# Kernel optimization log

Hardware: AMD Instinct MI355X
Metric: run time of the kernel (lower is better)

Reference implementation:

```python
import jax, jax.numpy as jnp
import numpy as np

B = 64            # number of graphs
NPG = 64          # nodes per graph (static; lengths are all equal here)
N = B * NPG       # total nodes = sum(lengths)
LT = 128          # max text tokens per node
LL = 32           # max labels per node
VOCAB = 50000
TOTAL_NUM = 100000
D = 256           # embedding_text == embedding_label == hidden_dimension
OUT = 1024


def setup_inputs() -> dict:
    key = jax.random.key(0)
    ks = jax.random.split(key, 12)
    return {
        "text_ids": jax.random.randint(ks[0], (N, LT), 0, VOCAB),
        "label_ids": jax.random.randint(ks[1], (N, LL), 0, TOTAL_NUM),
        "text_len": jax.random.randint(ks[2], (N,), 1, LT + 1),
        "label_len": jax.random.randint(ks[3], (N,), 1, LL + 1),
        "word_emb": jax.random.normal(ks[4], (VOCAB, D), jnp.float32) * 0.02,
        "label_emb": jax.random.normal(ks[5], (TOTAL_NUM, D), jnp.float32) * 0.02,
        "Wg_text": jax.random.normal(ks[6], (D, D), jnp.float32) * (1.0 / np.sqrt(D)),
        "Wg_label": jax.random.normal(ks[7], (D, D), jnp.float32) * (1.0 / np.sqrt(D)),
        "w_adap": jax.random.normal(ks[8], (2,), jnp.float32),
        "W1": jax.random.normal(ks[9], (D, D), jnp.float32) * (1.0 / np.sqrt(D)),
        "b1": jnp.zeros((D,), jnp.float32),
        "Wout": jax.random.normal(ks[10], (D, OUT), jnp.float32) * (1.0 / np.sqrt(D)),
        "bout": jnp.zeros((OUT,), jnp.float32),
    }


def _ragged_bag(table, ids, lens, mean):
    # gather rows then masked sum over the ragged axis (EmbeddingBag-style)
    L = ids.shape[1]
    mask = (jnp.arange(L)[None, :] < lens[:, None]).astype(table.dtype)  # [N, L]
    emb = table[ids]                                                     # [N, L, D]
    out = jnp.einsum("nld,nl->nd", emb, mask)
    if mean:
        out = out / lens[:, None].astype(table.dtype)
    return out


def reference(text_ids, label_ids, text_len, label_len, word_emb, label_emb,
              Wg_text, Wg_label, w_adap, W1, b1, Wout, bout):
    # fetchFeature: per-node ragged mean of word embeddings, ragged sum of label embeddings
    text_out = _ragged_bag(word_emb, text_ids, text_len, mean=True)    # [N, D]
    label_out = _ragged_bag(label_emb, label_ids, label_len, mean=False)  # [N, D]

    # weighted_GCN surrogate: per-type linear projection + relu, then per-graph mean readout
    h_t = jax.nn.relu(text_out @ Wg_text)   # [N, D]
    h_l = jax.nn.relu(label_out @ Wg_label)  # [N, D]
    seg = jnp.repeat(jnp.arange(B), NPG)     # graph id per node
    r_t = jax.ops.segment_sum(h_t, seg, num_segments=B) / NPG  # [B, D]
    r_l = jax.ops.segment_sum(h_l, seg, num_segments=B) / NPG  # [B, D]

    # adap: Linear(2,1,bias=False) over stacked (text,label), then MLLinear fusion
    fused = jnp.stack([r_t, r_l], axis=-1) @ w_adap  # [B, D]
    h = jax.nn.relu(fused @ W1 + b1)
    return h @ Wout + bout  # [B, OUT]
```

## Files before the change

### kernel.cpp

```cpp
#include <hip/hip_runtime.h>

#define NN      4096
#define BG      64
#define NPG_    64
#define LT_     128
#define LL_     32
#define D_      256
#define OUT_    1024

typedef __attribute__((ext_vector_type(8))) short bf16x8;
typedef __attribute__((ext_vector_type(4))) float f32x4;

__device__ __forceinline__ void split_bf16(float v, unsigned short& hi, unsigned short& lo) {
    union { float f; unsigned u; } a; a.f = v;
    const unsigned hu = (a.u + 0x8000u) & 0xFFFF0000u;
    union { unsigned u; float f; } h; h.u = hu;
    const float r = v - h.f;
    union { float f; unsigned u; } b; b.f = r;
    hi = (unsigned short)(hu >> 16);
    lo = (unsigned short)(((b.u + 0x8000u) & 0xFFFF0000u) >> 16);
}

__global__ __launch_bounds__(256) void convw_kernel(
    const float* __restrict__ Wg_text,
    const float* __restrict__ Wg_label,
    unsigned short* __restrict__ Wpk)
{
    const int b   = blockIdx.x;
    const int mat = b >> 7;
    const int nt  = (b >> 3) & 15;
    const int ks  = b & 7;
    const float* __restrict__ W = mat ? Wg_label : Wg_text;
    const int tid = threadIdx.x;

    #pragma unroll
    for (int r = 0; r < 2; ++r) {
        const int idx = tid + 256 * r;
        const int kl  = idx >> 4;
        const int c16 = idx & 15;
        const int k   = ks * 32 + kl;
        const float v = W[(size_t)k * D_ + nt * 16 + c16];
        unsigned short h, l;
        split_bf16(v, h, l);
        const int lane = c16 + 16 * ((kl >> 3) & 3);
        const int e    = kl & 7;
        const size_t bh = ((((size_t)mat * 2 + 0) * 16 + nt) * 8 + ks) * 512 + lane * 8 + e;
        const size_t bl = ((((size_t)mat * 2 + 1) * 16 + nt) * 8 + ks) * 512 + lane * 8 + e;
        Wpk[bh] = h;
        Wpk[bl] = l;
    }
}

__global__ __launch_bounds__(256) void gather_kernel(
    const int*   __restrict__ text_ids,
    const int*   __restrict__ label_ids,
    const int*   __restrict__ text_len,
    const int*   __restrict__ label_len,
    const float* __restrict__ word_emb,
    const float* __restrict__ label_emb,
    unsigned short* __restrict__ xh_t,
    unsigned short* __restrict__ xl_t,
    unsigned short* __restrict__ xh_l,
    unsigned short* __restrict__ xl_l)
{
    __shared__ int   sIds[LT_ + LL_];
    __shared__ float redT[4][D_];
    __shared__ float redL[4][D_];

    const int n    = blockIdx.x;
    const int tid  = threadIdx.x;
    const int wave = tid >> 6;
    const int lane = tid & 63;

    if (tid < LT_)               sIds[tid] = text_ids [(size_t)n * LT_ + tid];
    else if (tid < LT_ + LL_)    sIds[tid] = label_ids[(size_t)n * LL_ + (tid - LT_)];
    const int lt = text_len[n];
    const int ll = label_len[n];
    __syncthreads();

    float4 aT = make_float4(0.f, 0.f, 0.f, 0.f);
    float4 aL = make_float4(0.f, 0.f, 0.f, 0.f);

    {
        const float* __restrict__ bp = word_emb + (size_t)lane * 4;
        #pragma unroll 8
        for (int l = wave; l < lt; l += 4) {
            const float4 v = *reinterpret_cast<const float4*>(bp + (size_t)sIds[l] * D_);
            aT.x += v.x; aT.y += v.y; aT.z += v.z; aT.w += v.w;
        }
    }
    {
        const float* __restrict__ bp = label_emb + (size_t)lane * 4;
        #pragma unroll 8
        for (int l = wave; l < ll; l += 4) {
            const float4 v = *reinterpret_cast<const float4*>(bp + (size_t)sIds[LT_ + l] * D_);
            aL.x += v.x; aL.y += v.y; aL.z += v.z; aL.w += v.w;
        }
    }

    *reinterpret_cast<float4*>(&redT[wave][lane * 4]) = aT;
    *reinterpret_cast<float4*>(&redL[wave][lane * 4]) = aL;
    __syncthreads();

    const float t  = ((redT[0][tid] + redT[1][tid]) + (redT[2][tid] + redT[3][tid])) / (float)lt;
    const float lv =  (redL[0][tid] + redL[1][tid]) + (redL[2][tid] + redL[3][tid]);

    unsigned short h, l;
    const size_t o = (size_t)n * D_ + tid;
    split_bf16(t,  h, l);  xh_t[o] = h;  xl_t[o] = l;
    split_bf16(lv, h, l);  xh_l[o] = h;  xl_l[o] = l;
}

__global__ __launch_bounds__(512) void proj_kernel(
    const unsigned short* __restrict__ xh_t,
    const unsigned short* __restrict__ xl_t,
    const unsigned short* __restrict__ xh_l,
    const unsigned short* __restrict__ xl_l,
    const unsigned short* __restrict__ Wpk,
    const float* __restrict__ w_adap,
    float*       __restrict__ h_comb)
{
    __shared__ __align__(16) short ldsX[4][16 * D_];

    const int tid  = threadIdx.x;
    const int wave = tid >> 6;
    const int lane = tid & 63;
    const int base = blockIdx.x * 16;

    {
        const int nd = tid >> 5, ch = tid & 31;
        const size_t g = (size_t)(base + nd) * D_ + ch * 8;
        const int d = nd * D_ + ((ch ^ (nd & 7)) * 8);
        *reinterpret_cast<int4*>(&ldsX[0][d]) = *reinterpret_cast<const int4*>(&xh_t[g]);
        *reinterpret_cast<int4*>(&ldsX[1][d]) = *reinterpret_cast<const int4*>(&xl_t[g]);
        *reinterpret_cast<int4*>(&ldsX[2][d]) = *reinterpret_cast<const int4*>(&xh_l[g]);
        *reinterpret_cast<int4*>(&ldsX[3][d]) = *reinterpret_cast<const int4*>(&xl_l[g]);
    }
    __syncthreads();

    const int nt0 = wave * 2;
    const int row = lane & 15;
    const int kc  = lane >> 4;
    f32x4 accT[2] = {{0.f,0.f,0.f,0.f},{0.f,0.f,0.f,0.f}};
    f32x4 accL[2] = {{0.f,0.f,0.f,0.f},{0.f,0.f,0.f,0.f}};

    #pragma unroll
    for (int ks = 0; ks < 8; ++ks) {
        const int aidx = row * D_ + (((ks * 4 + kc) ^ (row & 7)) * 8);
        const bf16x8 ath  = *reinterpret_cast<const bf16x8*>(&ldsX[0][aidx]);
        const bf16x8 atl  = *reinterpret_cast<const bf16x8*>(&ldsX[1][aidx]);
        const bf16x8 alh  = *reinterpret_cast<const bf16x8*>(&ldsX[2][aidx]);
        const bf16x8 all_ = *reinterpret_cast<const bf16x8*>(&ldsX[3][aidx]);

        #pragma unroll
        for (int i = 0; i < 2; ++i) {
            const int nt = nt0 + i;
            const bf16x8 bth = *reinterpret_cast<const bf16x8*>(
                &Wpk[(((size_t)0 * 16 + nt) * 8 + ks) * 512 + lane * 8]);
            const bf16x8 btl = *reinterpret_cast<const bf16x8*>(
                &Wpk[(((size_t)1 * 16 + nt) * 8 + ks) * 512 + lane * 8]);
            const bf16x8 blh = *reinterpret_cast<const bf16x8*>(
                &Wpk[(((size_t)2 * 16 + nt) * 8 + ks) * 512 + lane * 8]);
            const bf16x8 bll = *reinterpret_cast<const bf16x8*>(
                &Wpk[(((size_t)3 * 16 + nt) * 8 + ks) * 512 + lane * 8]);

            accT[i] = __builtin_amdgcn_mfma_f32_16x16x32_bf16(ath, bth, accT[i], 0, 0, 0);
            accT[i] = __builtin_amdgcn_mfma_f32_16x16x32_bf16(ath, btl, accT[i], 0, 0, 0);
            accT[i] = __builtin_amdgcn_mfma_f32_16x16x32_bf16(atl, bth, accT[i], 0, 0, 0);
            accT[i] = __builtin_amdgcn_mfma_f32_16x16x32_bf16(atl, btl, accT[i], 0, 0, 0);

            accL[i] = __builtin_amdgcn_mfma_f32_16x16x32_bf16(alh, blh, accL[i], 0, 0, 0);
            accL[i] = __builtin_amdgcn_mfma_f32_16x16x32_bf16(alh, bll, accL[i], 0, 0, 0);
            accL[i] = __builtin_amdgcn_mfma_f32_16x16x32_bf16(all_, blh, accL[i], 0, 0, 0);
            accL[i] = __builtin_amdgcn_mfma_f32_16x16x32_bf16(all_, bll, accL[i], 0, 0, 0);
        }
    }

    const float w0r = w_adap[0] * (1.0f / (float)NPG_);
    const float w1r = w_adap[1] * (1.0f / (float)NPG_);
    #pragma unroll
    for (int i = 0; i < 2; ++i) {
        #pragma unroll
        for (int r = 0; r < 4; ++r) {
            const int node = base + kc * 4 + r;
            const int col  = (nt0 + i) * 16 + row;
            const float ht = accT[i][r] > 0.f ? accT[i][r] : 0.f;
            const float hl = accL[i][r] > 0.f ? accL[i][r] : 0.f;
            h_comb[(size_t)node * D_ + col] = w0r * ht + w1r * hl;
        }
    }
}

__global__ __launch_bounds__(256) void graph_kernel(
    const float* __restrict__ h_comb,
    const float* __restrict__ W1,
    const float* __restrict__ b1,
    const float* __restrict__ Wout,
    const float* __restrict__ bout,
    float*       __restrict__ out)
{
    __shared__ float fused[D_];
    __shared__ float hrow[D_];

    const int bx   = blockIdx.x;
    const int b    = bx >> 2;
    const int part = bx & 3;
    const int tid  = threadIdx.x;

    float acc = 0.f;
    const float* __restrict__ basep = h_comb + (size_t)b * NPG_ * D_ + tid;
    #pragma unroll 8
    for (int n = 0; n < NPG_; ++n) acc += basep[(size_t)n * D_];
    fused[tid] = acc;
    __syncthreads();

    float a1 = b1[tid];
    for (int d = 0; d < D_; ++d)
        a1 = fmaf(fused[d], W1[(size_t)d * D_ + tid], a1);
    hrow[tid] = a1 > 0.f ? a1 : 0.f;
    __syncthreads();

    const int j = part * 256 + tid;
    float o = bout[j];
    for (int d = 0; d < D_; ++d)
        o = fmaf(hrow[d], Wout[(size_t)d * OUT_ + j], o);
    out[(size_t)b * OUT_ + j] = o;
}

extern "C" void kernel_launch(void* const* d_in, const int* in_sizes, int n_in,
                              void* d_out, int out_size, void* d_ws, size_t ws_size,
                              hipStream_t stream) {
    const int*   text_ids  = (const int*)  d_in[0];
    const int*   label_ids = (const int*)  d_in[1];
    const int*   text_len  = (const int*)  d_in[2];
    const int*   label_len = (const int*)  d_in[3];
    const float* word_emb  = (const float*)d_in[4];
    const float* label_emb = (const float*)d_in[5];
    const float* Wg_text   = (const float*)d_in[6];
    const float* Wg_label  = (const float*)d_in[7];
    const float* w_adap    = (const float*)d_in[8];
    const float* W1        = (const float*)d_in[9];
    const float* b1        = (const float*)d_in[10];
    const float* Wout      = (const float*)d_in[11];
    const float* bout      = (const float*)d_in[12];

    char* ws = (char*)d_ws;
    float*          h_comb = (float*)ws;
    unsigned short* xh_t   = (unsigned short*)(ws + (4  << 20));
    unsigned short* xl_t   = (unsigned short*)(ws + (6  << 20));
    unsigned short* xh_l   = (unsigned short*)(ws + (8  << 20));
    unsigned short* xl_l   = (unsigned short*)(ws + (10 << 20));
    unsigned short* Wpk    = (unsigned short*)(ws + (12 << 20));
    float*          out    = (float*)d_out;

    convw_kernel<<<256, 256, 0, stream>>>(Wg_text, Wg_label, Wpk);

    gather_kernel<<<NN, 256, 0, stream>>>(
        text_ids, label_ids, text_len, label_len,
        word_emb, label_emb, xh_t, xl_t, xh_l, xl_l);

    proj_kernel<<<NN / 16, 512, 0, stream>>>(
        xh_t, xl_t, xh_l, xl_l, Wpk, w_adap, h_comb);

    graph_kernel<<<BG * 4, 256, 0, stream>>>(
        h_comb, W1, b1, Wout, bout, out);
}
```

Baseline: 88.83 us.

## Split proj kernel across column halves and drop low-low MFMA term

The projection kernel now launches twice as many blocks, each covering half the output columns with one 16-column tile per wave instead of two, which raises parallelism across CUs. It also removes the lo*lo product from the split-bf16 three-term emulation, cutting the MFMAs per tile from 8 to 6. A min-blocks hint is added to launch bounds. Each block still reloads the full 16-node input tile into LDS, so input reads double. Dropping the lo*lo term slightly reduces precision.

```diff
diff --git a/kernel.cpp b/kernel.cpp
--- a/kernel.cpp
+++ b/kernel.cpp
@@ -111,7 +111,7 @@
     split_bf16(lv, h, l);  xh_l[o] = h;  xl_l[o] = l;
 }
 
-__global__ __launch_bounds__(512) void proj_kernel(
+__global__ __launch_bounds__(512, 4) void proj_kernel(
     const unsigned short* __restrict__ xh_t,
     const unsigned short* __restrict__ xl_t,
     const unsigned short* __restrict__ xh_l,
@@ -122,10 +122,12 @@
 {
     __shared__ __align__(16) short ldsX[4][16 * D_];
 
-    const int tid  = threadIdx.x;
-    const int wave = tid >> 6;
-    const int lane = tid & 63;
-    const int base = blockIdx.x * 16;
+    const int tid   = threadIdx.x;
+    const int wave  = tid >> 6;
+    const int lane  = tid & 63;
+    const int ntile = blockIdx.x >> 1;
+    const int chalf = blockIdx.x & 1;
+    const int base  = ntile * 16;
 
     {
         const int nd = tid >> 5, ch = tid & 31;
@@ -138,11 +140,11 @@
     }
     __syncthreads();
 
-    const int nt0 = wave * 2;
+    const int nt  = chalf * 8 + wave;
     const int row = lane & 15;
     const int kc  = lane >> 4;
-    f32x4 accT[2] = {{0.f,0.f,0.f,0.f},{0.f,0.f,0.f,0.f}};
-    f32x4 accL[2] = {{0.f,0.f,0.f,0.f},{0.f,0.f,0.f,0.f}};
+    f32x4 accT = {0.f, 0.f, 0.f, 0.f};
+    f32x4 accL = {0.f, 0.f, 0.f, 0.f};
 
     #pragma unroll
     for (int ks = 0; ks < 8; ++ks) {
@@ -152,42 +154,33 @@
         const bf16x8 alh  = *reinterpret_cast<const bf16x8*>(&ldsX[2][aidx]);
         const bf16x8 all_ = *reinterpret_cast<const bf16x8*>(&ldsX[3][aidx]);
 
-        #pragma unroll
-        for (int i = 0; i < 2; ++i) {
-            const int nt = nt0 + i;
-            const bf16x8 bth = *reinterpret_cast<const bf16x8*>(
-                &Wpk[(((size_t)0 * 16 + nt) * 8 + ks) * 512 + lane * 8]);
-            const bf16x8 btl = *reinterpret_cast<const bf16x8*>(
-                &Wpk[(((size_t)1 * 16 + nt) * 8 + ks) * 512 + lane * 8]);
-            const bf16x8 blh = *reinterpret_cast<const bf16x8*>(
-                &Wpk[(((size_t)2 * 16 + nt) * 8 + ks) * 512 + lane * 8]);
-            const bf16x8 bll = *reinterpret_cast<const bf16x8*>(
-                &Wpk[(((size_t)3 * 16 + nt) * 8 + ks) * 512 + lane * 8]);
-
-            accT[i] = __builtin_amdgcn_mfma_f32_16x16x32_bf16(ath, bth, accT[i], 0, 0, 0);
-            accT[i] = __builtin_amdgcn_mfma_f32_16x16x32_bf16(ath, btl, accT[i], 0, 0, 0);
-            accT[i] = __builtin_amdgcn_mfma_f32_16x16x32_bf16(atl, bth, accT[i], 0, 0, 0);
-            accT[i] = __builtin_amdgcn_mfma_f32_16x16x32_bf16(atl, btl, accT[i], 0, 0, 0);
-
-            accL[i] = __builtin_amdgcn_mfma_f32_16x16x32_bf16(alh, blh, accL[i], 0, 0, 0);
-            accL[i] = __builtin_amdgcn_mfma_f32_16x16x32_bf16(alh, bll, accL[i], 0, 0, 0);
-            accL[i] = __builtin_amdgcn_mfma_f32_16x16x32_bf16(all_, blh, accL[i], 0, 0, 0);
-            accL[i] = __builtin_amdgcn_mfma_f32_16x16x32_bf16(all_, bll, accL[i], 0, 0, 0);
-        }
+        const bf16x8 bth = *reinterpret_cast<const bf16x8*>(
+            &Wpk[(((size_t)0 * 16 + nt) * 8 + ks) * 512 + lane * 8]);
+        const bf16x8 btl = *reinterpret_cast<const bf16x8*>(
+            &Wpk[(((size_t)1 * 16 + nt) * 8 + ks) * 512 + lane * 8]);
+        const bf16x8 blh = *reinterpret_cast<const bf16x8*>(
+            &Wpk[(((size_t)2 * 16 + nt) * 8 + ks) * 512 + lane * 8]);
+        const bf16x8 bll = *reinterpret_cast<const bf16x8*>(
+            &Wpk[(((size_t)3 * 16 + nt) * 8 + ks) * 512 + lane * 8]);
+
+        accT = __builtin_amdgcn_mfma_f32_16x16x32_bf16(ath, bth, accT, 0, 0, 0);
+        accT = __builtin_amdgcn_mfma_f32_16x16x32_bf16(ath, btl, accT, 0, 0, 0);
+        accT = __builtin_amdgcn_mfma_f32_16x16x32_bf16(atl, bth, accT, 0, 0, 0);
+
+        accL = __builtin_amdgcn_mfma_f32_16x16x32_bf16(alh, blh, accL, 0, 0, 0);
+        accL = __builtin_amdgcn_mfma_f32_16x16x32_bf16(alh, bll, accL, 0, 0, 0);
+        accL = __builtin_amdgcn_mfma_f32_16x16x32_bf16(all_, blh, accL, 0, 0, 0);
     }
 
     const float w0r = w_adap[0] * (1.0f / (float)NPG_);
     const float w1r = w_adap[1] * (1.0f / (float)NPG_);
     #pragma unroll
-    for (int i = 0; i < 2; ++i) {
-        #pragma unroll
-        for (int r = 0; r < 4; ++r) {
-            const int node = base + kc * 4 + r;
-            const int col  = (nt0 + i) * 16 + row;
-            const float ht = accT[i][r] > 0.f ? accT[i][r] : 0.f;
-            const float hl = accL[i][r] > 0.f ? accL[i][r] : 0.f;
-            h_comb[(size_t)node * D_ + col] = w0r * ht + w1r * hl;
-        }
+    for (int r = 0; r < 4; ++r) {
+        const int node = base + kc * 4 + r;
+        const int col  = nt * 16 + row;
+        const float ht = accT[r] > 0.f ? accT[r] : 0.f;
+        const float hl = accL[r] > 0.f ? accL[r] : 0.f;
+        h_comb[(size_t)node * D_ + col] = w0r * ht + w1r * hl;
     }
 }
 
@@ -259,7 +252,7 @@
         text_ids, label_ids, text_len, label_len,
         word_emb, label_emb, xh_t, xl_t, xh_l, xl_l);
 
-    proj_kernel<<<NN / 16, 512, 0, stream>>>(
+    proj_kernel<<<NN / 16 * 2, 512, 0, stream>>>(
         xh_t, xl_t, xh_l, xl_l, Wpk, w_adap, h_comb);
 
     graph_kernel<<<BG * 4, 256, 0, stream>>>(
```

Result: no change. 87.58 us (-1.4%).
